# Optimization experiments

Measured on AMD Instinct MI355X. Metric: run time of the kernel, lower is better.

The kernel has to match this reference:

```python
import jax, jax.numpy as jnp
import numpy as np

B, C, H, W = 4, 256, 64, 64
E = C // 8  # embedding_channels = inChannels // k


def setup_inputs() -> dict:
    key = jax.random.key(0)
    ks = jax.random.split(key, 9)
    sc = 1.0 / np.sqrt(C)
    so = 1.0 / np.sqrt(E)
    return {
        "x": jax.random.normal(ks[0], (B, C, H, W), dtype=jnp.float32),
        "Wk": jax.random.normal(ks[1], (E, C), dtype=jnp.float32) * sc,
        "bk": jax.random.normal(ks[2], (E,), dtype=jnp.float32) * 0.01,
        "Wq": jax.random.normal(ks[3], (E, C), dtype=jnp.float32) * sc,
        "bq": jax.random.normal(ks[4], (E,), dtype=jnp.float32) * 0.01,
        "Wv": jax.random.normal(ks[5], (E, C), dtype=jnp.float32) * sc,
        "bv": jax.random.normal(ks[6], (E,), dtype=jnp.float32) * 0.01,
        "Wo": jax.random.normal(ks[7], (C, E), dtype=jnp.float32) * so,
        "bo": jax.random.normal(ks[8], (C,), dtype=jnp.float32) * 0.01,
    }


def reference(x, Wk, bk, Wq, bq, Wv, bv, Wo, bo):
    b, c, h, w = x.shape
    n = h * w
    gamma = jnp.float32(0.5)  # non-learned branch (learned=False default)

    def conv1x1(inp, Wt, bt):
        # 1x1 conv == channel-mixing matmul: [b,c,h,w] x [e,c] -> [b,e,h,w]
        return jnp.einsum('bchw,ec->behw', inp, Wt) + bt[None, :, None, None]

    f = conv1x1(x, Wk, bk).reshape(b, -1, n)  # key   [b,E,N]
    g = conv1x1(x, Wq, bq).reshape(b, -1, n)  # query [b,E,N]
    hx = conv1x1(x, Wv, bv).reshape(b, -1, n)  # value [b,E,N]

    s = jnp.einsum('bei,bej->bij', f, g)       # f^T @ g, [b,N,N]
    beta = jax.nn.softmax(s, axis=1)           # softmax over dim 1 (rows) as in torch
    v = jnp.einsum('bei,bij->bej', hx, beta)   # h @ beta, [b,E,N]
    v = v.reshape(b, -1, h, w)

    o = jnp.einsum('behw,ce->bchw', v, Wo) + bo[None, :, None, None]
    y = gamma * o + x
    return y, o, gamma
```

## Files before the change

### kernel.cpp

```cpp
#include <hip/hip_runtime.h>

#define B_ 4
#define C_ 256
#define N_ 4096
#define E_ 32

typedef _Float16 f16x8 __attribute__((ext_vector_type(8)));
typedef _Float16 f16x4 __attribute__((ext_vector_type(4)));
typedef _Float16 f16x2 __attribute__((ext_vector_type(2)));
typedef float f32x4 __attribute__((ext_vector_type(4)));
typedef float f32x2 __attribute__((ext_vector_type(2)));

#define LOG2E 1.44269504088896f

__global__ __launch_bounds__(256) void proj_kernel(
    const float* __restrict__ x,
    const float* __restrict__ Wk, const float* __restrict__ bk,
    const float* __restrict__ Wq, const float* __restrict__ bq,
    const float* __restrict__ Wv, const float* __restrict__ bv,
    _Float16* __restrict__ Qb, _Float16* __restrict__ Kb, _Float16* __restrict__ Vb)
{
    const int m   = blockIdx.x >> 8;
    const int rem = blockIdx.x & 255;
    const int b   = rem >> 6;
    const int n0  = (rem & 63) << 6;
    const int t    = threadIdx.x;
    const int lane = t & 63;
    const int wave = t >> 6;
    const int l15  = lane & 15;
    const int quad = lane >> 4;

    __shared__ _Float16 xT[64][264];
    __shared__ _Float16 Wl[32][264];

    const float* W    = (m == 0) ? Wk : (m == 1) ? Wq : Wv;
    const float* bias = (m == 0) ? bk : (m == 1) ? bq : bv;

    for (int i4 = t; i4 < (E_ * C_) / 4; i4 += 256) {
        float4 wv = ((const float4*)W)[i4];
        int e = (i4 * 4) >> 8, c = (i4 * 4) & 255;
        f16x4 tp = {(_Float16)wv.x, (_Float16)wv.y, (_Float16)wv.z, (_Float16)wv.w};
        *(f16x4*)&Wl[e][c] = tp;
    }
    for (int i4 = t; i4 < (64 * 256) / 4; i4 += 256) {
        int j4 = (i4 & 15) * 4;
        int c  = i4 >> 4;
        float4 xv = *(const float4*)(x + (size_t)(b * C_ + c) * N_ + n0 + j4);
        xT[j4 + 0][c] = (_Float16)xv.x;
        xT[j4 + 1][c] = (_Float16)xv.y;
        xT[j4 + 2][c] = (_Float16)xv.z;
        xT[j4 + 3][c] = (_Float16)xv.w;
    }
    __syncthreads();

    f16x8 Bf[8];
    for (int kk = 0; kk < 8; ++kk)
        Bf[kk] = *(const f16x8*)&xT[wave * 16 + l15][kk * 32 + quad * 8];

    const float sc = (m == 1) ? LOG2E : 1.0f;
    for (int et = 0; et < 2; ++et) {
        f32x4 acc = {0.f, 0.f, 0.f, 0.f};
        for (int kk = 0; kk < 8; ++kk) {
            f16x8 Af = *(const f16x8*)&Wl[et * 16 + l15][kk * 32 + quad * 8];
            acc = __builtin_amdgcn_mfma_f32_16x16x32_f16(Af, Bf[kk], acc, 0, 0, 0);
        }
        const int n = n0 + wave * 16 + l15;
        for (int r = 0; r < 4; ++r) {
            const int e = et * 16 + quad * 4 + r;
            float v = (acc[r] + bias[e]) * sc;
            _Float16 hv = (_Float16)v;
            if      (m == 0) Kb[(size_t)(b * N_ + n) * E_ + e] = hv;
            else if (m == 1) Qb[(size_t)(b * N_ + n) * E_ + e] = hv;
            else             Vb[(size_t)(b * E_ + e) * N_ + n] = hv;
        }
    }
}

__global__ __launch_bounds__(512, 4) void attn_kernel(
    const _Float16* __restrict__ Qb, const _Float16* __restrict__ Kb,
    const _Float16* __restrict__ Vb, _Float16* __restrict__ Ob)
{
    const int wave = threadIdx.x >> 6;
    const int lane = threadIdx.x & 63;
    const int l15  = lane & 15, quad = lane >> 4;
    const int jg   = blockIdx.x;
    const int b    = jg >> 8;
    const int j0   = (jg & 255) << 4;

    __shared__ _Float16 pb[8][16][136];
    __shared__ float    osum[8][16][36];
    __shared__ float    mls[8][2][16];

    f16x8 Qf = *(const f16x8*)(Qb + (size_t)(b * N_ + j0 + l15) * E_ + quad * 8);

    f32x4 O0 = {0, 0, 0, 0}, O1 = {0, 0, 0, 0};
    float mrow = -1e30f, lsum = 0.f;

    const _Float16* Kbase = Kb + (size_t)b * N_ * E_;
    const _Float16* Vbase = Vb + (size_t)b * E_ * N_;
    const int ibase = wave << 9;

    f16x8 Kf[8];
    for (int s = 0; s < 8; ++s)
        Kf[s] = *(const f16x8*)(Kbase + (size_t)(ibase + s * 16 + l15) * E_ + quad * 8);

    for (int it = 0; it < 4; ++it) {
        const int i0 = ibase + it * 128;
        f32x4 S[8];
        for (int s = 0; s < 8; ++s) {
            f32x4 z = {0, 0, 0, 0};
            S[s] = __builtin_amdgcn_mfma_f32_16x16x32_f16(Kf[s], Qf, z, 0, 0, 0);
        }
        float t0, t1, t2, t3;
        t0 = fmaxf(fmaxf(S[0][0], S[0][1]), fmaxf(S[0][2], S[0][3]));
        t1 = fmaxf(fmaxf(S[1][0], S[1][1]), fmaxf(S[1][2], S[1][3]));
        t2 = fmaxf(fmaxf(S[2][0], S[2][1]), fmaxf(S[2][2], S[2][3]));
        t3 = fmaxf(fmaxf(S[3][0], S[3][1]), fmaxf(S[3][2], S[3][3]));
        float mA = fmaxf(fmaxf(t0, t1), fmaxf(t2, t3));
        t0 = fmaxf(fmaxf(S[4][0], S[4][1]), fmaxf(S[4][2], S[4][3]));
        t1 = fmaxf(fmaxf(S[5][0], S[5][1]), fmaxf(S[5][2], S[5][3]));
        t2 = fmaxf(fmaxf(S[6][0], S[6][1]), fmaxf(S[6][2], S[6][3]));
        t3 = fmaxf(fmaxf(S[7][0], S[7][1]), fmaxf(S[7][2], S[7][3]));
        float mx = fmaxf(mA, fmaxf(fmaxf(t0, t1), fmaxf(t2, t3)));
        mx = fmaxf(mx, __shfl_xor(mx, 16));
        mx = fmaxf(mx, __shfl_xor(mx, 32));
        float mnew  = fmaxf(mrow, mx);
        float alpha = exp2f(mrow - mnew);
        mrow = mnew;
        float ss[8];
        for (int s = 0; s < 8; ++s) {
            float p0 = exp2f(S[s][0] - mnew);
            float p1 = exp2f(S[s][1] - mnew);
            float p2 = exp2f(S[s][2] - mnew);
            float p3 = exp2f(S[s][3] - mnew);
            S[s][0] = p0; S[s][1] = p1; S[s][2] = p2; S[s][3] = p3;
            ss[s] = (p0 + p1) + (p2 + p3);
        }
        float ps = ((ss[0] + ss[1]) + (ss[2] + ss[3]))
                 + ((ss[4] + ss[5]) + (ss[6] + ss[7]));
        lsum = lsum * alpha + ps;
        for (int r = 0; r < 4; ++r) { O0[r] *= alpha; O1[r] *= alpha; }
        for (int s = 0; s < 8; ++s) {
            f16x4 tp = {(_Float16)S[s][0], (_Float16)S[s][1],
                        (_Float16)S[s][2], (_Float16)S[s][3]};
            *(f16x4*)&pb[wave][l15][s * 16 + quad * 4] = tp;
        }
        f16x8 P[4];
        for (int kc = 0; kc < 4; ++kc)
            P[kc] = *(const f16x8*)&pb[wave][l15][kc * 32 + quad * 8];
        f16x8 Va[4], Vc[4];
        for (int kc = 0; kc < 4; ++kc) {
            Va[kc] = *(const f16x8*)(Vbase + (size_t)l15 * N_ + i0 + kc * 32 + quad * 8);
            Vc[kc] = *(const f16x8*)(Vbase + (size_t)(16 + l15) * N_ + i0 + kc * 32 + quad * 8);
        }
        const int inext = (it < 3) ? (i0 + 128) : ibase;
        for (int s = 0; s < 8; ++s)
            Kf[s] = *(const f16x8*)(Kbase + (size_t)(inext + s * 16 + l15) * E_ + quad * 8);
        for (int kc = 0; kc < 4; ++kc) {
            O0 = __builtin_amdgcn_mfma_f32_16x16x32_f16(Va[kc], P[kc], O0, 0, 0, 0);
            O1 = __builtin_amdgcn_mfma_f32_16x16x32_f16(Vc[kc], P[kc], O1, 0, 0, 0);
        }
    }

    lsum += __shfl_xor(lsum, 16);
    lsum += __shfl_xor(lsum, 32);
    if (quad == 0) { mls[wave][0][l15] = mrow; mls[wave][1][l15] = lsum; }
    __syncthreads();

    float M = -1e30f, ms[8], ls[8];
    for (int s = 0; s < 8; ++s) {
        ms[s] = mls[s][0][l15]; ls[s] = mls[s][1][l15];
        M = fmaxf(M, ms[s]);
    }
    float L = 0.f;
    for (int s = 0; s < 8; ++s) L += ls[s] * exp2f(ms[s] - M);
    const float w = exp2f(mrow - M) / L;

    *(f32x4*)&osum[wave][l15][quad * 4]      = O0 * w;
    *(f32x4*)&osum[wave][l15][16 + quad * 4] = O1 * w;
    __syncthreads();

    const int j = threadIdx.x >> 5;
    const int e = threadIdx.x & 31;
    float a = 0.f;
    for (int s = 0; s < 8; ++s)
        a += osum[s][j][e];
    Ob[(size_t)(b * N_ + j0 + j) * E_ + e] = (_Float16)a;
}

__global__ __launch_bounds__(256) void out_kernel(
    const _Float16* __restrict__ Ob, const float* __restrict__ Wo,
    const float* __restrict__ bo, const float* __restrict__ x,
    float* __restrict__ out)
{
    const int bi  = blockIdx.x;
    const int b   = bi >> 8;
    const int rem = bi & 255;
    const int n0  = (rem >> 2) << 6;
    const int cq  = rem & 3;
    const int t = threadIdx.x, lane = t & 63, wave = t >> 6;
    const int l15 = lane & 15, quad = lane >> 4;

    __shared__ _Float16 Wl[64][40];
    for (int i4 = t; i4 < (64 * E_) / 4; i4 += 256) {
        int c = (i4 * 4) >> 5, e = (i4 * 4) & 31;
        float4 wv = *(const float4*)(Wo + (size_t)(cq * 64 + c) * E_ + e);
        f16x4 tp = {(_Float16)wv.x, (_Float16)wv.y, (_Float16)wv.z, (_Float16)wv.w};
        *(f16x4*)&Wl[c][e] = tp;
    }
    __syncthreads();

    const int nloc = wave * 16 + l15;
    f16x8 Bf = *(const f16x8*)(Ob + (size_t)(b * N_ + n0 + nloc) * E_ + quad * 8);

    float* out_y = out;
    float* out_o = out + (size_t)B_ * C_ * N_;

    for (int tt = 0; tt < 4; ++tt) {
        f16x8 Af = *(const f16x8*)&Wl[tt * 16 + l15][quad * 8];
        f32x4 z = {0, 0, 0, 0};
        f32x4 acc = __builtin_amdgcn_mfma_f32_16x16x32_f16(Af, Bf, z, 0, 0, 0);
        for (int r = 0; r < 4; ++r) {
            const int c = cq * 64 + tt * 16 + quad * 4 + r;
            size_t idx = (size_t)(b * C_ + c) * N_ + n0 + nloc;
            float ov = acc[r] + bo[c];
            out_o[idx] = ov;
            out_y[idx] = 0.5f * ov + x[idx];
        }
    }
    if (bi == 0 && t == 0)
        out[(size_t)2 * B_ * C_ * N_] = 0.5f;
}

extern "C" void kernel_launch(void* const* d_in, const int* in_sizes, int n_in,
                              void* d_out, int out_size, void* d_ws, size_t ws_size,
                              hipStream_t stream)
{
    const float* x  = (const float*)d_in[0];
    const float* Wk = (const float*)d_in[1];
    const float* bk = (const float*)d_in[2];
    const float* Wq = (const float*)d_in[3];
    const float* bq = (const float*)d_in[4];
    const float* Wv = (const float*)d_in[5];
    const float* bv = (const float*)d_in[6];
    const float* Wo = (const float*)d_in[7];
    const float* bo = (const float*)d_in[8];
    float* out = (float*)d_out;

    char* ws = (char*)d_ws;
    _Float16* Qb = (_Float16*)(ws);
    _Float16* Kb = (_Float16*)(ws + (1u << 20));
    _Float16* Vb = (_Float16*)(ws + (2u << 20));
    _Float16* Ob = (_Float16*)(ws + (3u << 20));

    proj_kernel<<<dim3(3 * B_ * (N_ / 64)), dim3(256), 0, stream>>>(
        x, Wk, bk, Wq, bq, Wv, bv, Qb, Kb, Vb);
    attn_kernel<<<dim3(B_ * (N_ / 16)), dim3(512), 0, stream>>>(
        Qb, Kb, Vb, Ob);
    out_kernel <<<dim3(4 * B_ * (N_ / 64)), dim3(256), 0, stream>>>(
        Ob, Wo, bo, x, out);
}
```

Baseline: 150.4 us.

## Fuse output projection and residual into attention epilogue, drop out_kernel

The output 1x1 projection, bias, residual add and gamma write move into the end of the attention kernel. The per-block 16x32 attention result is reduced into shared memory and multiplied by an fp16 copy of Wo, which extra blocks of the projection kernel now prepare. This removes one kernel launch and the global round trip of the intermediate attention output. In exchange, each block stores only 16-element (64-byte) contiguous segments per channel, and 256 extra blocks redundantly convert the same Wo. The shared-memory paddings for pb and osum also shrink, which changes bank mapping and leaves some vector LDS accesses misaligned.

```diff
diff --git a/kernel.cpp b/kernel.cpp
--- a/kernel.cpp
+++ b/kernel.cpp
@@ -7,9 +7,7 @@
 
 typedef _Float16 f16x8 __attribute__((ext_vector_type(8)));
 typedef _Float16 f16x4 __attribute__((ext_vector_type(4)));
-typedef _Float16 f16x2 __attribute__((ext_vector_type(2)));
 typedef float f32x4 __attribute__((ext_vector_type(4)));
-typedef float f32x2 __attribute__((ext_vector_type(2)));
 
 #define LOG2E 1.44269504088896f
 
@@ -18,9 +16,21 @@
     const float* __restrict__ Wk, const float* __restrict__ bk,
     const float* __restrict__ Wq, const float* __restrict__ bq,
     const float* __restrict__ Wv, const float* __restrict__ bv,
-    _Float16* __restrict__ Qb, _Float16* __restrict__ Kb, _Float16* __restrict__ Vb)
+    const float* __restrict__ Wo,
+    _Float16* __restrict__ Qb, _Float16* __restrict__ Kb, _Float16* __restrict__ Vb,
+    _Float16* __restrict__ Wof16, float* __restrict__ out)
 {
-    const int m   = blockIdx.x >> 8;
+    const int m = blockIdx.x >> 8;
+    if (m == 3) {
+        for (int i4 = threadIdx.x; i4 < (C_ * E_) / 4; i4 += 256) {
+            float4 wv = ((const float4*)Wo)[i4];
+            f16x4 tp = {(_Float16)wv.x, (_Float16)wv.y, (_Float16)wv.z, (_Float16)wv.w};
+            *(f16x4*)&Wof16[i4 * 4] = tp;
+        }
+        if (threadIdx.x == 0)
+            out[(size_t)2 * B_ * C_ * N_] = 0.5f;
+        return;
+    }
     const int rem = blockIdx.x & 255;
     const int b   = rem >> 6;
     const int n0  = (rem & 63) << 6;
@@ -78,7 +88,9 @@
 
 __global__ __launch_bounds__(512, 4) void attn_kernel(
     const _Float16* __restrict__ Qb, const _Float16* __restrict__ Kb,
-    const _Float16* __restrict__ Vb, _Float16* __restrict__ Ob)
+    const _Float16* __restrict__ Vb, const _Float16* __restrict__ Wof16,
+    const float* __restrict__ bo, const float* __restrict__ x,
+    float* __restrict__ out)
 {
     const int wave = threadIdx.x >> 6;
     const int lane = threadIdx.x & 63;
@@ -87,9 +99,10 @@
     const int b    = jg >> 8;
     const int j0   = (jg & 255) << 4;
 
-    __shared__ _Float16 pb[8][16][136];
-    __shared__ float    osum[8][16][36];
+    __shared__ _Float16 pb[8][16][132];
+    __shared__ float    osum[8][16][34];
     __shared__ float    mls[8][2][16];
+    __shared__ _Float16 Om[16][36];
 
     f16x8 Qf = *(const f16x8*)(Qb + (size_t)(b * N_ + j0 + l15) * E_ + quad * 8);
 
@@ -180,56 +193,32 @@
     *(f32x4*)&osum[wave][l15][16 + quad * 4] = O1 * w;
     __syncthreads();
 
-    const int j = threadIdx.x >> 5;
-    const int e = threadIdx.x & 31;
-    float a = 0.f;
-    for (int s = 0; s < 8; ++s)
-        a += osum[s][j][e];
-    Ob[(size_t)(b * N_ + j0 + j) * E_ + e] = (_Float16)a;
-}
-
-__global__ __launch_bounds__(256) void out_kernel(
-    const _Float16* __restrict__ Ob, const float* __restrict__ Wo,
-    const float* __restrict__ bo, const float* __restrict__ x,
-    float* __restrict__ out)
-{
-    const int bi  = blockIdx.x;
-    const int b   = bi >> 8;
-    const int rem = bi & 255;
-    const int n0  = (rem >> 2) << 6;
-    const int cq  = rem & 3;
-    const int t = threadIdx.x, lane = t & 63, wave = t >> 6;
-    const int l15 = lane & 15, quad = lane >> 4;
-
-    __shared__ _Float16 Wl[64][40];
-    for (int i4 = t; i4 < (64 * E_) / 4; i4 += 256) {
-        int c = (i4 * 4) >> 5, e = (i4 * 4) & 31;
-        float4 wv = *(const float4*)(Wo + (size_t)(cq * 64 + c) * E_ + e);
-        f16x4 tp = {(_Float16)wv.x, (_Float16)wv.y, (_Float16)wv.z, (_Float16)wv.w};
-        *(f16x4*)&Wl[c][e] = tp;
-    }
-    __syncthreads();
-
-    const int nloc = wave * 16 + l15;
-    f16x8 Bf = *(const f16x8*)(Ob + (size_t)(b * N_ + n0 + nloc) * E_ + quad * 8);
-
-    float* out_y = out;
-    float* out_o = out + (size_t)B_ * C_ * N_;
-
-    for (int tt = 0; tt < 4; ++tt) {
-        f16x8 Af = *(const f16x8*)&Wl[tt * 16 + l15][quad * 8];
+    {
+        const int j = threadIdx.x >> 5;
+        const int e = threadIdx.x & 31;
+        float a = 0.f;
+        for (int s = 0; s < 8; ++s) a += osum[s][j][e];
+        Om[j][e] = (_Float16)a;
+    }
+    __syncthreads();
+
+    f16x8 Bf2 = *(const f16x8*)&Om[l15][quad * 8];
+    float* out_y = out + (size_t)b * C_ * N_;
+    float* out_o = out + (size_t)B_ * C_ * N_ + (size_t)b * C_ * N_;
+    const float* xb = x + (size_t)b * C_ * N_;
+    for (int ct = 0; ct < 2; ++ct) {
+        const int c0 = wave * 32 + ct * 16;
+        f16x8 Af = *(const f16x8*)(Wof16 + (size_t)(c0 + l15) * E_ + quad * 8);
         f32x4 z = {0, 0, 0, 0};
-        f32x4 acc = __builtin_amdgcn_mfma_f32_16x16x32_f16(Af, Bf, z, 0, 0, 0);
+        f32x4 acc = __builtin_amdgcn_mfma_f32_16x16x32_f16(Af, Bf2, z, 0, 0, 0);
         for (int r = 0; r < 4; ++r) {
-            const int c = cq * 64 + tt * 16 + quad * 4 + r;
-            size_t idx = (size_t)(b * C_ + c) * N_ + n0 + nloc;
+            const int c = c0 + quad * 4 + r;
+            size_t idx = (size_t)c * N_ + j0 + l15;
             float ov = acc[r] + bo[c];
             out_o[idx] = ov;
-            out_y[idx] = 0.5f * ov + x[idx];
-        }
-    }
-    if (bi == 0 && t == 0)
-        out[(size_t)2 * B_ * C_ * N_] = 0.5f;
+            out_y[idx] = 0.5f * ov + xb[idx];
+        }
+    }
 }
 
 extern "C" void kernel_launch(void* const* d_in, const int* in_sizes, int n_in,
@@ -248,15 +237,13 @@
     float* out = (float*)d_out;
 
     char* ws = (char*)d_ws;
-    _Float16* Qb = (_Float16*)(ws);
-    _Float16* Kb = (_Float16*)(ws + (1u << 20));
-    _Float16* Vb = (_Float16*)(ws + (2u << 20));
-    _Float16* Ob = (_Float16*)(ws + (3u << 20));
-
-    proj_kernel<<<dim3(3 * B_ * (N_ / 64)), dim3(256), 0, stream>>>(
-        x, Wk, bk, Wq, bq, Wv, bv, Qb, Kb, Vb);
+    _Float16* Qb    = (_Float16*)(ws);
+    _Float16* Kb    = (_Float16*)(ws + (1u << 20));
+    _Float16* Vb    = (_Float16*)(ws + (2u << 20));
+    _Float16* Wof16 = (_Float16*)(ws + (3u << 20));
+
+    proj_kernel<<<dim3(3 * B_ * (N_ / 64) + 256), dim3(256), 0, stream>>>(
+        x, Wk, bk, Wq, bq, Wv, bv, Wo, Qb, Kb, Vb, Wof16, out);
     attn_kernel<<<dim3(B_ * (N_ / 16)), dim3(512), 0, stream>>>(
-        Qb, Kb, Vb, Ob);
-    out_kernel <<<dim3(4 * B_ * (N_ / 64)), dim3(256), 0, stream>>>(
-        Ob, Wo, bo, x, out);
+        Qb, Kb, Vb, Wof16, bo, x, out);
 }
```

Result: no change. 149.0 us (-0.9%).
